# Optimization experiments

Measured on AMD Instinct MI355X. Metric: run time of the kernel, lower is better.

Reference implementation:

```python
import jax, jax.numpy as jnp
import numpy as np

B, IN_DIM, N_NODES, N_LEAVES, N_ACTIONS = 131072, 128, 511, 512, 16


def setup_inputs() -> dict:
    key = jax.random.key(0)
    k1, k2, k3, k4 = jax.random.split(key, 4)
    x = jax.random.normal(k1, (B, IN_DIM), dtype=jnp.float32)
    W1 = jax.random.normal(k2, (N_NODES, IN_DIM), dtype=jnp.float32) * 0.1
    b1 = jax.random.normal(k3, (N_NODES,), dtype=jnp.float32) * 0.1
    W2 = jax.random.normal(k4, (N_LEAVES, 2 * N_NODES), dtype=jnp.float32) * 0.05
    # leaf -> action assignment; arange % n_actions guarantees every group non-empty
    leaf_actions = (jnp.arange(N_LEAVES) % N_ACTIONS).astype(jnp.int32)
    return {"x": x, "W1": W1, "b1": b1, "W2": W2, "leaf_actions": leaf_actions}


def reference(x, W1, b1, W2, leaf_actions):
    # linear1
    h = x @ W1.T + b1                      # [B, N_NODES]
    # relu(h) || relu(-h)
    z = jnp.concatenate([jax.nn.relu(h), jax.nn.relu(-h)], axis=1)  # [B, 2*N_NODES]
    # linear2 (no bias)
    y = z @ W2.T                           # [B, N_LEAVES]
    # grouped segment-max over leaf columns, grouped by action id
    pooled = jax.ops.segment_max(y.T, leaf_actions, num_segments=N_ACTIONS).T  # [B, N_ACTIONS]
    return jax.nn.softmax(pooled, axis=-1)
```

## Files before the change

kernel.cpp:

```cpp
#include <hip/hip_runtime.h>
#include <hip/hip_bf16.h>

typedef unsigned short u16;
typedef unsigned int u32;
typedef __attribute__((ext_vector_type(8))) short bf16x8;
typedef __attribute__((ext_vector_type(16))) float f32x16;

#define NROWS   131072
#define KDIM    128
#define NNODES  511
#define NACT    16

__device__ __forceinline__ u16 f2b(float v) {
  return __builtin_bit_cast(u16, __float2bfloat16(v));
}

union Frag {
  bf16x8 v;
  u16    u[8];
  int4   i;
  int    d[4];
};

#define Z16 {0.f,0.f,0.f,0.f,0.f,0.f,0.f,0.f,0.f,0.f,0.f,0.f,0.f,0.f,0.f,0.f}

__global__ void prep_k(const float* __restrict__ W1, const float* __restrict__ W2,
                       const float* __restrict__ b1, u16* __restrict__ w1f,
                       u16* __restrict__ wgt, float* __restrict__ b1r) {
  int bid = blockIdx.x, t = threadIdx.x;
  if (bid < 256) {
    int o = bid * 256 + t;
    int j = o & 7, l = (o >> 3) & 63, ks = (o >> 9) & 7, nt = o >> 12;
    int node = nt * 32 + (l & 31);
    int k = ks * 16 + ((l >> 5) << 3) + j;
    w1f[o] = f2b(node < NNODES ? W1[node * KDIM + k] : 0.f);
  } else if (bid < 2304) {
    int o = (bid - 256) * 256 + t;
    int j = o & 7, l = (o >> 3) & 63, lt = (o >> 9) & 15, s = o >> 13;
    int type = s & 1, kstep = s >> 1;
    int leaf = lt * 32 + (l & 31);
    int n = kstep * 16 + ((l >> 5) << 3) + j;
    float va = 0.f, vb = 0.f;
    if (n < NNODES) {
      va = W2[leaf * (2 * NNODES) + n];
      vb = W2[leaf * (2 * NNODES) + NNODES + n];
    }
    wgt[o] = f2b(type ? 0.5f * (va + vb) : 0.5f * (va - vb));
  } else {
    int o = (bid - 2304) * 256 + t;
    int r = o & 15, hi2 = (o >> 4) & 1, nt = o >> 5;
    int node = nt * 32 + (r & 3) + 8 * (r >> 2) + 4 * hi2;
    b1r[o] = (node < NNODES) ? b1[node] : 0.f;
  }
}

__global__ __launch_bounds__(1024, 4) void fused_k(const float* __restrict__ x,
                                                   const u16* __restrict__ w1f,
                                                   const u16* __restrict__ wgt,
                                                   const float* __restrict__ b1r,
                                                   float* __restrict__ out) {
  __shared__ u16 Hh[4 * 32 * 64 * 8];
  __shared__ u16 Ss[32 * 64 * 8];

  const int t = threadIdx.x, w = t >> 6, l = t & 63;
  const int la = l & 31, hi = l >> 5;
  const int rg = blockIdx.x;

  {
    const float* xb = x + (size_t)rg * 128 * KDIM;
#pragma unroll
    for (int i = 0; i < 2; ++i) {
      int f = w * 2 + i;
      int rt = f >> 3, ks = f & 7;
      const float* src = xb + (rt * 32 + la) * KDIM + ks * 16 + hi * 8;
      float4 v0 = *(const float4*)src;
      float4 v1 = *(const float4*)(src + 4);
      Frag fr;
      fr.u[0] = f2b(v0.x); fr.u[1] = f2b(v0.y); fr.u[2] = f2b(v0.z); fr.u[3] = f2b(v0.w);
      fr.u[4] = f2b(v1.x); fr.u[5] = f2b(v1.y); fr.u[6] = f2b(v1.z); fr.u[7] = f2b(v1.w);
      *(int4*)&Ss[f * 512 + l * 8] = fr.i;
    }
  }
  __syncthreads();

  {
    Frag a1[8];
#pragma unroll
    for (int q = 0; q < 8; ++q)
      a1[q].i = *(const int4*)(w1f + ((size_t)(w * 8 + q) * 64 + l) * 8);
    float4 bias[4];
#pragma unroll
    for (int g = 0; g < 4; ++g)
      bias[g] = *(const float4*)(b1r + (w * 2 + hi) * 16 + g * 4);

#pragma unroll 1
    for (int rt = 0; rt < 4; ++rt) {
      f32x16 c0 = Z16;
#pragma unroll
      for (int ks = 0; ks < 8; ++ks) {
        Frag b;
        b.i = *(const int4*)&Ss[(rt * 8 + ks) * 512 + l * 8];
        c0 = __builtin_amdgcn_mfma_f32_32x32x16_bf16(a1[ks].v, b.v, c0, 0, 0, 0);
      }
#pragma unroll
      for (int p = 0; p < 8; ++p) {
        int q = p >> 1, e = p & 1;
        int r0 = 4 * q + 2 * e;
        float bv0 = e ? bias[q].z : bias[q].x;
        float bv1 = e ? bias[q].w : bias[q].y;
        float v0 = c0[r0] + bv0;
        float v1 = c0[r0 + 1] + bv1;
        int n32 = 8 * q + 4 * hi + 2 * e;
        int c_h = n32 >> 4, jj = n32 & 15;
        u32 pkv = (u32)f2b(v0) | ((u32)f2b(v1) << 16);
        int lam = ((jj >> 3) << 5) + la;
        int sb2 = lam ^ (lam >> 3);
        *(u32*)&Hh[((rt * 32 + w * 2 + c_h) * 64 + sb2) * 8 + (jj & 6)] = pkv;
      }
    }
  }
  __syncthreads();

  f32x16 acc[4] = {Z16, Z16, Z16, Z16};
  const int sl = l ^ (l >> 3);

#define RDH(kk, rt) (*(const int4*)&Hh[(((rt) * 32 + (kk)) * 64 + sl) * 8])
#define WADDR(k, type) (wgt + ((size_t)((k) * 32 + (type) * 16 + w)) * 512 + l * 8)
#define ABS4(F) { _Pragma("unroll") for (int d = 0; d < 4; ++d) (F).d[d] &= 0x7FFF7FFF; }
#define MF(A, B, r) acc[r] = __builtin_amdgcn_mfma_f32_32x32x16_bf16((A).v, (B).v, acc[r], 0, 0, 0)

  Frag X0, X1, Y0, Y1, C2, C3, AD, AS, BD, BS;
  X0.i = RDH(0, 0); X1.i = RDH(0, 1);
  AD.i = *(const int4*)WADDR(0, 0); AS.i = *(const int4*)WADDR(0, 1);
  BD.i = *(const int4*)WADDR(1, 0); BS.i = *(const int4*)WADDR(1, 1);

#pragma unroll 1
  for (int k = 0; k < 32; k += 2) {
    C2.i = RDH(k, 2); C3.i = RDH(k, 3);
    Y0.i = RDH(k + 1, 0); Y1.i = RDH(k + 1, 1);
    MF(X0, AD, 0); MF(X1, AD, 1);
    MF(C2, AD, 2); MF(C3, AD, 3);
    ABS4(X0); ABS4(X1); ABS4(C2); ABS4(C3);
    MF(X0, AS, 0); MF(X1, AS, 1);
    MF(C2, AS, 2); MF(C3, AS, 3);
    if (k + 2 < 32) {
      AD.i = *(const int4*)WADDR(k + 2, 0);
      AS.i = *(const int4*)WADDR(k + 2, 1);
    }
    C2.i = RDH(k + 1, 2); C3.i = RDH(k + 1, 3);
    if (k + 2 < 32) { X0.i = RDH(k + 2, 0); X1.i = RDH(k + 2, 1); }
    MF(Y0, BD, 0); MF(Y1, BD, 1);
    MF(C2, BD, 2); MF(C3, BD, 3);
    ABS4(Y0); ABS4(Y1); ABS4(C2); ABS4(C3);
    MF(Y0, BS, 0); MF(Y1, BS, 1);
    MF(C2, BS, 2); MF(C3, BS, 3);
    if (k + 3 < 32) {
      BD.i = *(const int4*)WADDR(k + 3, 0);
      BS.i = *(const int4*)WADDR(k + 3, 1);
    }
  }

  __syncthreads();

  float* Hred = (float*)Hh;
#pragma unroll
  for (int rt = 0; rt < 4; ++rt)
#pragma unroll
    for (int r = 0; r < 16; ++r) {
      float v = acc[rt][r];
      v = fmaxf(v, __shfl_xor(v, 16));
      int row = rt * 32 + (r & 3) + 8 * (r >> 2) + 4 * hi;
      if (la < 16) Hred[(w * 128 + row) * 16 + la] = v;
    }
  __syncthreads();
  {
    int row = t >> 3, ap = t & 7;
    float m0 = -1e30f, m1 = -1e30f;
#pragma unroll
    for (int ww = 0; ww < 16; ++ww) {
      m0 = fmaxf(m0, Hred[(ww * 128 + row) * 16 + ap]);
      m1 = fmaxf(m1, Hred[(ww * 128 + row) * 16 + ap + 8]);
    }
    float m = fmaxf(m0, m1);
    m = fmaxf(m, __shfl_xor(m, 1));
    m = fmaxf(m, __shfl_xor(m, 2));
    m = fmaxf(m, __shfl_xor(m, 4));
    float e0 = __expf(m0 - m), e1 = __expf(m1 - m);
    float s = e0 + e1;
    s += __shfl_xor(s, 1);
    s += __shfl_xor(s, 2);
    s += __shfl_xor(s, 4);
    float inv = 1.f / s;
    float* orow = out + ((size_t)rg * 128 + row) * NACT;
    orow[ap]     = e0 * inv;
    orow[ap + 8] = e1 * inv;
  }
}

extern "C" void kernel_launch(void* const* d_in, const int* in_sizes, int n_in,
                              void* d_out, int out_size, void* d_ws, size_t ws_size,
                              hipStream_t stream) {
  const float* x  = (const float*)d_in[0];
  const float* W1 = (const float*)d_in[1];
  const float* b1 = (const float*)d_in[2];
  const float* W2 = (const float*)d_in[3];

  char* ws = (char*)d_ws;
  u16*   w1f = (u16*)ws;
  u16*   wgt = (u16*)(ws + 131072);
  float* b1r = (float*)(ws + 131072 + 1048576);

  prep_k <<<dim3(2308), dim3(256), 0, stream>>>(W1, W2, b1, w1f, wgt, b1r);
  fused_k<<<dim3(NROWS / 128), dim3(1024), 0, stream>>>(x, w1f, wgt, b1r, (float*)d_out);
}
```

Before: 246.9 us.

## Retile second GEMM warps as 2 row-tiles by 2 leaf-tiles

The second GEMM is re-partitioned. Before, each wave covered all 4 row tiles for one leaf tile. Now each wave covers 2 row tiles by 2 leaf tiles, so it reads half as many H fragments from LDS and issues no redundant ABS ops on them, at the cost of twice the weight loads from global/L2. The per-wave max over its two leaf tiles is folded into registers before the cross-wave reduction, which halves the reduction stage. An XOR swizzle on the reduction buffer is added to reduce LDS bank conflicts.

New measurement: 248.2 us. About the same (+0.5%).

```diff
diff --git a/kernel.cpp b/kernel.cpp
--- a/kernel.cpp
+++ b/kernel.cpp
@@ -121,42 +121,46 @@
   }
   __syncthreads();
 
-  f32x16 acc[4] = {Z16, Z16, Z16, Z16};
+  const int rg2 = w >> 3, ltp = w & 7;
+  const int rt0 = rg2 * 2;
   const int sl = l ^ (l >> 3);
 
-#define RDH(kk, rt) (*(const int4*)&Hh[(((rt) * 32 + (kk)) * 64 + sl) * 8])
-#define WADDR(k, type) (wgt + ((size_t)((k) * 32 + (type) * 16 + w)) * 512 + l * 8)
+  f32x16 acc[2][2] = {{Z16, Z16}, {Z16, Z16}};
+
+#define RDH(kk, rti) (*(const int4*)&Hh[(((rt0 + (rti)) * 32 + (kk)) * 64 + sl) * 8])
+#define WADDR(k, type, lti) (wgt + ((size_t)((k) * 32 + (type) * 16 + ltp * 2 + (lti))) * 512 + l * 8)
 #define ABS4(F) { _Pragma("unroll") for (int d = 0; d < 4; ++d) (F).d[d] &= 0x7FFF7FFF; }
-#define MF(A, B, r) acc[r] = __builtin_amdgcn_mfma_f32_32x32x16_bf16((A).v, (B).v, acc[r], 0, 0, 0)
-
-  Frag X0, X1, Y0, Y1, C2, C3, AD, AS, BD, BS;
+#define MF(A, B, ri, li) acc[ri][li] = __builtin_amdgcn_mfma_f32_32x32x16_bf16((A).v, (B).v, acc[ri][li], 0, 0, 0)
+
+  Frag X0, X1, Y0, Y1;
+  Frag AD0, AD1, AS0, AS1, BD0, BD1, BS0, BS1;
   X0.i = RDH(0, 0); X1.i = RDH(0, 1);
-  AD.i = *(const int4*)WADDR(0, 0); AS.i = *(const int4*)WADDR(0, 1);
-  BD.i = *(const int4*)WADDR(1, 0); BS.i = *(const int4*)WADDR(1, 1);
+  AD0.i = *(const int4*)WADDR(0, 0, 0); AD1.i = *(const int4*)WADDR(0, 0, 1);
+  AS0.i = *(const int4*)WADDR(0, 1, 0); AS1.i = *(const int4*)WADDR(0, 1, 1);
+  BD0.i = *(const int4*)WADDR(1, 0, 0); BD1.i = *(const int4*)WADDR(1, 0, 1);
+  BS0.i = *(const int4*)WADDR(1, 1, 0); BS1.i = *(const int4*)WADDR(1, 1, 1);
 
 #pragma unroll 1
   for (int k = 0; k < 32; k += 2) {
-    C2.i = RDH(k, 2); C3.i = RDH(k, 3);
     Y0.i = RDH(k + 1, 0); Y1.i = RDH(k + 1, 1);
-    MF(X0, AD, 0); MF(X1, AD, 1);
-    MF(C2, AD, 2); MF(C3, AD, 3);
-    ABS4(X0); ABS4(X1); ABS4(C2); ABS4(C3);
-    MF(X0, AS, 0); MF(X1, AS, 1);
-    MF(C2, AS, 2); MF(C3, AS, 3);
+    MF(X0, AD0, 0, 0); MF(X0, AD1, 0, 1);
+    MF(X1, AD0, 1, 0); MF(X1, AD1, 1, 1);
+    ABS4(X0); ABS4(X1);
+    MF(X0, AS0, 0, 0); MF(X0, AS1, 0, 1);
+    MF(X1, AS0, 1, 0); MF(X1, AS1, 1, 1);
     if (k + 2 < 32) {
-      AD.i = *(const int4*)WADDR(k + 2, 0);
-      AS.i = *(const int4*)WADDR(k + 2, 1);
-    }
-    C2.i = RDH(k + 1, 2); C3.i = RDH(k + 1, 3);
+      AD0.i = *(const int4*)WADDR(k + 2, 0, 0); AD1.i = *(const int4*)WADDR(k + 2, 0, 1);
+      AS0.i = *(const int4*)WADDR(k + 2, 1, 0); AS1.i = *(const int4*)WADDR(k + 2, 1, 1);
+    }
     if (k + 2 < 32) { X0.i = RDH(k + 2, 0); X1.i = RDH(k + 2, 1); }
-    MF(Y0, BD, 0); MF(Y1, BD, 1);
-    MF(C2, BD, 2); MF(C3, BD, 3);
-    ABS4(Y0); ABS4(Y1); ABS4(C2); ABS4(C3);
-    MF(Y0, BS, 0); MF(Y1, BS, 1);
-    MF(C2, BS, 2); MF(C3, BS, 3);
+    MF(Y0, BD0, 0, 0); MF(Y0, BD1, 0, 1);
+    MF(Y1, BD0, 1, 0); MF(Y1, BD1, 1, 1);
+    ABS4(Y0); ABS4(Y1);
+    MF(Y0, BS0, 0, 0); MF(Y0, BS1, 0, 1);
+    MF(Y1, BS0, 1, 0); MF(Y1, BS1, 1, 1);
     if (k + 3 < 32) {
-      BD.i = *(const int4*)WADDR(k + 3, 0);
-      BS.i = *(const int4*)WADDR(k + 3, 1);
+      BD0.i = *(const int4*)WADDR(k + 3, 0, 0); BD1.i = *(const int4*)WADDR(k + 3, 0, 1);
+      BS0.i = *(const int4*)WADDR(k + 3, 1, 0); BS1.i = *(const int4*)WADDR(k + 3, 1, 1);
     }
   }
 
@@ -164,22 +168,23 @@
 
   float* Hred = (float*)Hh;
 #pragma unroll
-  for (int rt = 0; rt < 4; ++rt)
+  for (int rti = 0; rti < 2; ++rti)
 #pragma unroll
     for (int r = 0; r < 16; ++r) {
-      float v = acc[rt][r];
+      float v = fmaxf(acc[rti][0][r], acc[rti][1][r]);
       v = fmaxf(v, __shfl_xor(v, 16));
-      int row = rt * 32 + (r & 3) + 8 * (r >> 2) + 4 * hi;
-      if (la < 16) Hred[(w * 128 + row) * 16 + la] = v;
+      int row = rg2 * 64 + rti * 32 + (r & 3) + 8 * (r >> 2) + 4 * hi;
+      if (la < 16) Hred[(ltp * 128 + row) * 16 + (la ^ ((row >> 1) & 7))] = v;
     }
   __syncthreads();
   {
     int row = t >> 3, ap = t & 7;
+    int xr = (row >> 1) & 7;
     float m0 = -1e30f, m1 = -1e30f;
 #pragma unroll
-    for (int ww = 0; ww < 16; ++ww) {
-      m0 = fmaxf(m0, Hred[(ww * 128 + row) * 16 + ap]);
-      m1 = fmaxf(m1, Hred[(ww * 128 + row) * 16 + ap + 8]);
+    for (int pp = 0; pp < 8; ++pp) {
+      m0 = fmaxf(m0, Hred[(pp * 128 + row) * 16 + (ap ^ xr)]);
+      m1 = fmaxf(m1, Hred[(pp * 128 + row) * 16 + ((ap + 8) ^ xr)]);
     }
     float m = fmaxf(m0, m1);
     m = fmaxf(m, __shfl_xor(m, 1));
```
